# Kernel tuning notes

Measured on AMD Instinct MI355X. Metric: run time of the kernel, lower is better.

Reference implementation:

```python
import jax, jax.numpy as jnp
import numpy as np

D_MODEL = 768
N_HEAD = 12
N_KV_HEADS = 4
HEAD_DIM = D_MODEL // N_HEAD
N_REPEAT = N_HEAD // N_KV_HEADS
ROPE_BASE = 10000.0


def _rotate_half(x):
    # Faithful to the torch impl: reshape(..., 2, d/2) -> transpose(-2,-1) -> reshape
    # (interleaves the two halves), then chunk and cat(-x2, x1).
    d = x.shape[-1]
    xh = x.reshape(*x.shape[:-1], 2, d // 2).swapaxes(-2, -1).reshape(x.shape)
    x1, x2 = jnp.split(xh, 2, axis=-1)
    return jnp.concatenate([-x2, x1], axis=-1)


def _rope(x, pos):
    # x: [B, h, T, d], pos: [T] int
    d = x.shape[-1]
    inv_freq = 1.0 / (ROPE_BASE ** (jnp.arange(0, d, 2, dtype=jnp.float32) / d))
    freqs = pos.astype(jnp.float32)[:, None] * inv_freq[None, :]      # [T, d/2]
    emb = jnp.concatenate([freqs, freqs], axis=-1)                     # [T, d]
    cos = jnp.cos(emb)[None, None]                                     # [1,1,T,d]
    sin = jnp.sin(emb)[None, None]
    xf = x.astype(jnp.float32)
    return (xf * cos + _rotate_half(xf) * sin).astype(x.dtype)


def setup_inputs() -> dict:
    key = jax.random.key(0)
    ks = jax.random.split(key, 6)
    B, T, C = 8, 1024, D_MODEL
    s = 0.02
    return {
        "x": jax.random.normal(ks[0], (B, T, C), dtype=jnp.float32),
        "pos": jnp.arange(T, dtype=jnp.int32),
        "q_w": jax.random.normal(ks[1], (C, N_HEAD * HEAD_DIM), dtype=jnp.float32) * s,
        "q_b": jnp.zeros((N_HEAD * HEAD_DIM,), dtype=jnp.float32),
        "k_w": jax.random.normal(ks[2], (C, N_KV_HEADS * HEAD_DIM), dtype=jnp.float32) * s,
        "k_b": jnp.zeros((N_KV_HEADS * HEAD_DIM,), dtype=jnp.float32),
        "v_w": jax.random.normal(ks[3], (C, N_KV_HEADS * HEAD_DIM), dtype=jnp.float32) * s,
        "v_b": jnp.zeros((N_KV_HEADS * HEAD_DIM,), dtype=jnp.float32),
        "o_w": jax.random.normal(ks[4], (C, C), dtype=jnp.float32) * s,
        "o_b": jnp.zeros((C,), dtype=jnp.float32),
    }


def reference(x, pos, q_w, q_b, k_w, k_b, v_w, v_b, o_w, o_b):
    B, T, C = x.shape
    hd, H, KVH, rep = HEAD_DIM, N_HEAD, N_KV_HEADS, N_REPEAT

    Q = (x @ q_w + q_b).reshape(B, T, H, hd).transpose(0, 2, 1, 3)     # [B,H,T,hd]
    K = (x @ k_w + k_b).reshape(B, T, KVH, hd).transpose(0, 2, 1, 3)   # [B,KVH,T,hd]
    V = (x @ v_w + v_b).reshape(B, T, KVH, hd).transpose(0, 2, 1, 3)

    Q = _rope(Q, pos)
    K = _rope(K, pos)

    # Grouped attention: avoid materializing repeated KV (equiv. to repeat_interleave).
    Qg = Q.reshape(B, KVH, rep, T, hd)
    scores = jnp.einsum("bgrtd,bgsd->bgrts", Qg, K) / np.sqrt(hd).astype(np.float32)
    causal = jnp.tril(jnp.ones((T, T), dtype=bool))
    scores = jnp.where(causal, scores, jnp.finfo(scores.dtype).min)
    probs = jax.nn.softmax(scores, axis=-1)
    out = jnp.einsum("bgrts,bgsd->bgrtd", probs, V)                    # [B,KVH,rep,T,hd]
    out = out.reshape(B, H, T, hd).transpose(0, 2, 1, 3).reshape(B, T, C)
    return out @ o_w + o_b
```

## Files before the change

kernel.cpp:

```cpp
#include <hip/hip_runtime.h>
#include <hip/hip_bf16.h>
#include <math.h>

#define BATCH 8
#define SEQ   1024
#define DM    768
#define NHEAD 12
#define KVH   4
#define HD    64
#define REP   3

#define QSCALE 0.18033688011112042f

typedef unsigned short u16;
typedef __attribute__((ext_vector_type(8))) __bf16 bf16x8;
typedef __attribute__((ext_vector_type(4))) float f32x4;
typedef __attribute__((ext_vector_type(4))) unsigned int u32x4;
typedef __attribute__((address_space(1))) const unsigned int gu32_c;
typedef __attribute__((address_space(3))) unsigned int su32;

__device__ __forceinline__ u16 f2bf(float f) {
    unsigned int u = __float_as_uint(f);
    u += 0x7fffu + ((u >> 16) & 1u);
    return (u16)(u >> 16);
}

__global__ __launch_bounds__(256) void cvt_x_k(
    const float* __restrict__ in, u16* __restrict__ o, int n4)
{
    const int i = blockIdx.x * 256 + threadIdx.x;
    if (i >= n4) return;
    const float4 v = ((const float4*)in)[i];
    ushort4 r;
    r.x = f2bf(v.x); r.y = f2bf(v.y); r.z = f2bf(v.z); r.w = f2bf(v.w);
    ((ushort4*)o)[i] = r;
}

__global__ __launch_bounds__(256) void cvt_wqkv_k(
    const float* __restrict__ qw, const float* __restrict__ kw,
    const float* __restrict__ vw, u16* __restrict__ wt)
{
    const int idx = blockIdx.x * 256 + threadIdx.x;
    if (idx >= 1280 * DM) return;
    const int k = idx % DM;
    const int n = idx / DM;
    float v;
    if (n < 768)       v = qw[(size_t)k * 768 + n] * QSCALE;
    else if (n < 1024) v = kw[(size_t)k * 256 + (n - 768)];
    else               v = vw[(size_t)k * 256 + (n - 1024)];
    wt[idx] = f2bf(v);
}

__global__ __launch_bounds__(256) void cvt_wo_k(
    const float* __restrict__ ow, u16* __restrict__ wt)
{
    const int idx = blockIdx.x * 256 + threadIdx.x;
    if (idx >= DM * DM) return;
    const int k = idx % DM;
    const int n = idx / DM;
    wt[idx] = f2bf(ow[(size_t)k * DM + n]);
}

__device__ __forceinline__ void gemm128_body(
    const u16* __restrict__ A, const u16* __restrict__ B,
    int m0, int n0, u16* As, u16* Bs, f32x4 acc[4][4])
{
    const int tid  = threadIdx.x;
    const int lane = tid & 63;
    const int wid  = tid >> 6;
    const int wr = wid >> 1, wc = wid & 1;
    const int lo = lane & 15, hi = lane >> 4;

    const f32x4 z = {0.f, 0.f, 0.f, 0.f};
    #pragma unroll
    for (int i = 0; i < 4; i++)
        #pragma unroll
        for (int j = 0; j < 4; j++)
            acc[i][j] = z;

    for (int kt = 0; kt < DM; kt += 32) {
        #pragma unroll
        for (int r = 0; r < 2; ++r) {
            const int idx  = r * 256 + tid;
            const int row  = idx >> 2;
            const int col  = (idx & 3) << 3;
            const int base = (r * 256 + wid * 64) * 8;
            __builtin_amdgcn_global_load_lds(
                (gu32_c*)&A[(size_t)(m0 + row) * DM + kt + col],
                (su32*)&As[base], 16, 0, 0);
            __builtin_amdgcn_global_load_lds(
                (gu32_c*)&B[(size_t)(n0 + row) * DM + kt + col],
                (su32*)&Bs[base], 16, 0, 0);
        }
        __syncthreads();
        bf16x8 af[4], bfr[4];
        #pragma unroll
        for (int i = 0; i < 4; i++) af[i]  = *(const bf16x8*)&As[(wr * 64 + i * 16 + lo) * 32 + hi * 8];
        #pragma unroll
        for (int j = 0; j < 4; j++) bfr[j] = *(const bf16x8*)&Bs[(wc * 64 + j * 16 + lo) * 32 + hi * 8];
        #pragma unroll
        for (int i = 0; i < 4; i++)
            #pragma unroll
            for (int j = 0; j < 4; j++)
                acc[i][j] = __builtin_amdgcn_mfma_f32_16x16x32_bf16(af[i], bfr[j], acc[i][j], 0, 0, 0);
        __syncthreads();
    }
}

__global__ __launch_bounds__(256) void gemm_qkv(
    const u16* __restrict__ xb, const u16* __restrict__ wt,
    const float* __restrict__ qb, const float* __restrict__ kb,
    const float* __restrict__ vb,
    u16* __restrict__ Q, u16* __restrict__ K, u16* __restrict__ Vt)
{
    __shared__ __align__(16) u16 As[128 * 32];
    __shared__ __align__(16) u16 Bs[128 * 32];
    const int id = (blockIdx.x & 7) * 80 + (blockIdx.x >> 3);
    const int m0 = (id / 10) * 128;
    const int n0 = (id % 10) * 128;
    f32x4 acc[4][4];
    gemm128_body(xb, wt, m0, n0, As, Bs, acc);

    const int tid = threadIdx.x;
    const int lane = tid & 63, wid = tid >> 6;
    const int wr = wid >> 1, wc = wid & 1;
    const int lo = lane & 15, hi = lane >> 4;

    #pragma unroll
    for (int j = 0; j < 4; j++) {
        const int n = n0 + wc * 64 + j * 16 + lo;
        if (n < 1024) {
            u16* outp; int nl, Hcnt; float bias;
            if (n < 768) { outp = Q; nl = n;       Hcnt = NHEAD; bias = qb[n] * QSCALE; }
            else         { outp = K; nl = n - 768; Hcnt = KVH;   bias = kb[nl]; }
            const int head = nl >> 6, d = nl & 63;
            #pragma unroll
            for (int i = 0; i < 4; i++) {
                #pragma unroll
                for (int r = 0; r < 4; r++) {
                    const int m = m0 + wr * 64 + i * 16 + hi * 4 + r;
                    const int b = m >> 10, t = m & 1023;
                    outp[(((size_t)(b * Hcnt + head)) * SEQ + t) * HD + d] =
                        f2bf(acc[i][j][r] + bias);
                }
            }
        } else {
            const int nl = n - 1024;
            const float bias = vb[nl];
            const int head = nl >> 6, d = nl & 63;
            #pragma unroll
            for (int i = 0; i < 4; i++) {
                ushort4 vs;
                vs.x = f2bf(acc[i][j][0] + bias);
                vs.y = f2bf(acc[i][j][1] + bias);
                vs.z = f2bf(acc[i][j][2] + bias);
                vs.w = f2bf(acc[i][j][3] + bias);
                const int m = m0 + wr * 64 + i * 16 + hi * 4;
                const int b = m >> 10, t = m & 1023;
                *(ushort4*)&Vt[(((size_t)(b * KVH + head)) * HD + d) * SEQ + t] = vs;
            }
        }
    }
}

__global__ __launch_bounds__(256) void gemm_oproj(
    const u16* __restrict__ Ab, const u16* __restrict__ wt,
    const float* __restrict__ ob, float* __restrict__ outp)
{
    __shared__ __align__(16) u16 As[128 * 32];
    __shared__ __align__(16) u16 Bs[128 * 32];
    const int id = (blockIdx.x & 7) * 48 + (blockIdx.x >> 3);
    const int m0 = (id / 6) * 128;
    const int n0 = (id % 6) * 128;
    f32x4 acc[4][4];
    gemm128_body(Ab, wt, m0, n0, As, Bs, acc);

    const int tid = threadIdx.x;
    const int lane = tid & 63, wid = tid >> 6;
    const int wr = wid >> 1, wc = wid & 1;
    const int lo = lane & 15, hi = lane >> 4;

    #pragma unroll
    for (int j = 0; j < 4; j++) {
        const int n = n0 + wc * 64 + j * 16 + lo;
        const float bias = ob[n];
        #pragma unroll
        for (int i = 0; i < 4; i++) {
            #pragma unroll
            for (int r = 0; r < 4; r++) {
                const int m = m0 + wr * 64 + i * 16 + hi * 4 + r;
                outp[(size_t)m * DM + n] = acc[i][j][r] + bias;
            }
        }
    }
}

__global__ __launch_bounds__(256) void rope_naive(
    const __hip_bfloat16* __restrict__ Qin, __hip_bfloat16* __restrict__ Qout,
    const __hip_bfloat16* __restrict__ Kin, __hip_bfloat16* __restrict__ Kout,
    const int* __restrict__ pos)
{
    const long long qrows = (long long)BATCH * NHEAD * SEQ;
    const long long krows = (long long)BATCH * KVH * SEQ;
    const long long gid = (long long)blockIdx.x * 256 + threadIdx.x;
    if (gid >= (qrows + krows) * 64) return;
    long long row = gid >> 6;
    const int j = (int)(gid & 63);
    const __hip_bfloat16* in; __hip_bfloat16* outb;
    if (row < qrows) { in = Qin; outb = Qout; }
    else             { in = Kin; outb = Kout; row -= qrows; }
    const int t = (int)(row & (SEQ - 1));

    float p;
    if (pos[1] == 1)                              p = (float)pos[t];
    else if (((const float*)pos)[1] == 1.0f)      p = ((const float*)pos)[t];
    else                                          p = (float)pos[2 * t];

    const float inv = exp2f(-(float)(j & 31) * (13.287712379549449f / 32.0f));
    float sv, cv;
    sincosf(p * inv, &sv, &cv);
    const int partner = (j & 1) * 32 + (j >> 1) + ((j < 32) ? 16 : -16);
    const float sign  = (j < 32) ? -1.0f : 1.0f;
    const float val  = __bfloat162float(in[row * HD + j]);
    const float pv   = __bfloat162float(in[row * HD + partner]);
    outb[row * HD + j] = __float2bfloat16(val * cv + sign * pv * sv);
}

__device__ __forceinline__ void strip_compute(
    const bf16x8& qf0, const bf16x8& qf1,
    const bf16x8& k0, const bf16x8& k1, const bf16x8& k2, const bf16x8& k3,
    const bf16x8* vv, bool diag, int msk0, int hi,
    float& m, float& l, f32x4* O)
{
    const f32x4 z = {0.f, 0.f, 0.f, 0.f};
    f32x4 a0 = z, a1 = z;
    __builtin_amdgcn_s_setprio(1);
    a0 = __builtin_amdgcn_mfma_f32_16x16x32_bf16(k0, qf0, a0, 0, 0, 0);
    a0 = __builtin_amdgcn_mfma_f32_16x16x32_bf16(k1, qf1, a0, 0, 0, 0);
    a1 = __builtin_amdgcn_mfma_f32_16x16x32_bf16(k2, qf0, a1, 0, 0, 0);
    a1 = __builtin_amdgcn_mfma_f32_16x16x32_bf16(k3, qf1, a1, 0, 0, 0);
    __builtin_amdgcn_s_setprio(0);

    float sc[8];
    #pragma unroll
    for (int e = 0; e < 8; ++e)
        sc[e] = (e < 4) ? a0[e & 3] : a1[e & 3];
    if (diag) {
        #pragma unroll
        for (int e = 0; e < 8; ++e) {
            const int srel = ((e >> 2) << 4) + (hi << 2) + (e & 3);
            if (srel > msk0) sc[e] = -3.0e38f;
        }
    }
    float pm = sc[0];
    #pragma unroll
    for (int e = 1; e < 8; ++e) pm = fmaxf(pm, sc[e]);

    if (!__all(pm - m <= 8.0f)) {
        float pr = fmaxf(pm, __shfl_xor(pm, 16));
        pr = fmaxf(pr, __shfl_xor(pr, 32));
        const float mn = fmaxf(m, pr);
        const float f = exp2f(m - mn);
        l *= f;
        #pragma unroll
        for (int r = 0; r < 4; ++r) {
            const float fr = __shfl(f, hi * 4 + r);
            #pragma unroll
            for (int dj = 0; dj < 4; ++dj) O[dj][r] *= fr;
        }
        m = mn;
    }

    union { u16 u[8]; bf16x8 v; } pu;
    float ps = 0.f;
    #pragma unroll
    for (int e = 0; e < 8; ++e) {
        const float p = exp2f(sc[e] - m);
        ps += p;
        pu.u[e] = f2bf(p);
    }
    l += ps;

    __builtin_amdgcn_s_setprio(1);
    #pragma unroll
    for (int dj = 0; dj < 4; ++dj)
        O[dj] = __builtin_amdgcn_mfma_f32_16x16x32_bf16(pu.v, vv[dj], O[dj], 0, 0, 0);
    __builtin_amdgcn_s_setprio(0);
}

__global__ __launch_bounds__(256, 2) void attn_mfma(
    const u16* __restrict__ Q, const u16* __restrict__ K,
    const u16* __restrict__ Vt, u16* __restrict__ outp)
{
    __shared__ __align__(16) u16 Ks[2][2048];
    __shared__ __align__(16) u16 Vs[2][2048];

    const int wg = (blockIdx.x & 7) * 96 + (blockIdx.x >> 3);
    const int bh = wg >> 3;
    const int c  = wg & 7;
    const int b  = bh / NHEAD, h = bh % NHEAD;
    const int g  = h / REP;
    const int wid  = threadIdx.x >> 6;
    const int lane = threadIdx.x & 63;
    const int lo = lane & 15, hi = lane >> 4;

    const int w    = c + (wid << 3);
    const int sA   = 63 - w, sB = w;
    const int dA   = sA >> 1, dB = sB >> 1;
    const int mskA = lo + ((sA & 1) << 4);
    const int mskB = lo + ((sB & 1) << 4);
    const int nstT = ((63 - c) >> 1) + 1;

    const u16* Kp = K  + (size_t)(b * KVH + g) * SEQ * HD;
    const u16* Vp = Vt + (size_t)(b * KVH + g) * SEQ * HD;

    const int jK = (wid << 6) + lane;
    const int sKoff = (jK ^ ((jK >> 3) & 7)) << 3;
    int vsoff[4];
    #pragma unroll
    for (int q = 0; q < 4; ++q) {
        const int dw  = (wid << 8) + (q << 6) + lane;
        const int R   = dw >> 4;
        const int wd  = dw & 15;
        const int c8p = wd >> 1, ii = wd & 1;
        const int sc8 = (c8p >> 1) + ((c8p & 1) << 2);
        vsoff[q] = (R << 10) + (((sc8 << 1) + ii) << 1);
    }

    const u16* QpA = Q + ((size_t)(b * NHEAD + h) * SEQ + (sA << 4)) * HD;
    const u16* QpB = Q + ((size_t)(b * NHEAD + h) * SEQ + (sB << 4)) * HD;
    const bf16x8 qA0 = *(const bf16x8*)&QpA[(size_t)lo * HD + hi * 8];
    const bf16x8 qA1 = *(const bf16x8*)&QpA[(size_t)lo * HD + 32 + hi * 8];
    const bf16x8 qB0 = *(const bf16x8*)&QpB[(size_t)lo * HD + hi * 8];
    const bf16x8 qB1 = *(const bf16x8*)&QpB[(size_t)lo * HD + 32 + hi * 8];

    const f32x4 z = {0.f, 0.f, 0.f, 0.f};
    f32x4 OA[4], OB[4];
    #pragma unroll
    for (int dj = 0; dj < 4; ++dj) { OA[dj] = z; OB[dj] = z; }
    float mA = -3.0e38f, lA = 0.f, mB = -3.0e38f, lB = 0.f;

    #define STAGE(st_, bf_) do {                                              \
        const int s0_ = (st_) << 5;                                           \
        __builtin_amdgcn_global_load_lds(                                     \
            (gu32_c*)(Kp + (s0_ << 6) + sKoff),                               \
            (su32*)&Ks[bf_][wid << 9], 16, 0, 0);                             \
        _Pragma("unroll")                                                     \
        for (int q_ = 0; q_ < 4; ++q_)                                        \
            __builtin_amdgcn_global_load_lds(                                 \
                (gu32_c*)(Vp + s0_ + vsoff[q_]),                              \
                (su32*)&Vs[bf_][(wid << 9) + (q_ << 7)], 4, 0, 0);            \
    } while (0)

    STAGE(0, 0);
    __syncthreads();

    const int xorK = lo & 7;
    for (int st = 0; st < nstT; ++st) {
        const int buf = st & 1;
        if (st + 1 < nstT) STAGE(st + 1, buf ^ 1);

        if (st <= dA) {
            const u16* kb_ = Ks[buf];
            const bf16x8 k0 = *(const bf16x8*)&kb_[((lo << 3) + (hi ^ xorK)) << 3];
            const bf16x8 k1 = *(const bf16x8*)&kb_[((lo << 3) + ((4 + hi) ^ xorK)) << 3];
            const bf16x8 k2 = *(const bf16x8*)&kb_[(((16 + lo) << 3) + (hi ^ xorK)) << 3];
            const bf16x8 k3 = *(const bf16x8*)&kb_[(((16 + lo) << 3) + ((4 + hi) ^ xorK)) << 3];
            bf16x8 vv[4];
            #pragma unroll
            for (int dj = 0; dj < 4; ++dj)
                vv[dj] = *(const bf16x8*)&Vs[buf][((dj * 16 + lo) << 5) + (hi << 3)];

            strip_compute(qA0, qA1, k0, k1, k2, k3, vv, st == dA, mskA, hi, mA, lA, OA);
            if (st <= dB)
                strip_compute(qB0, qB1, k0, k1, k2, k3, vv, st == dB, mskB, hi, mB, lB, OB);
        }
        __syncthreads();
    }
    #undef STAGE

    lA += __shfl_xor(lA, 16); lA += __shfl_xor(lA, 32);
    lB += __shfl_xor(lB, 16); lB += __shfl_xor(lB, 32);
    #pragma unroll
    for (int r = 0; r < 4; ++r) {
        const float liA = 1.0f / fmaxf(__shfl(lA, hi * 4 + r), 1e-37f);
        const float liB = 1.0f / fmaxf(__shfl(lB, hi * 4 + r), 1e-37f);
        const int tA = (sA << 4) + hi * 4 + r;
        const int tB = (sB << 4) + hi * 4 + r;
        #pragma unroll
        for (int dj = 0; dj < 4; ++dj) {
            outp[((size_t)(b * SEQ + tA)) * DM + h * HD + dj * 16 + lo] = f2bf(OA[dj][r] * liA);
            outp[((size_t)(b * SEQ + tB)) * DM + h * HD + dj * 16 + lo] = f2bf(OB[dj][r] * liB);
        }
    }
}

extern "C" void kernel_launch(void* const* d_in, const int* in_sizes, int n_in,
                              void* d_out, int out_size, void* d_ws, size_t ws_size,
                              hipStream_t stream) {
    const float* x   = (const float*)d_in[0];
    const int*   pos = (const int*)d_in[1];
    const float* qw  = (const float*)d_in[2];
    const float* qb  = (const float*)d_in[3];
    const float* kw  = (const float*)d_in[4];
    const float* kb  = (const float*)d_in[5];
    const float* vw  = (const float*)d_in[6];
    const float* vb  = (const float*)d_in[7];
    const float* ow  = (const float*)d_in[8];
    const float* ob  = (const float*)d_in[9];
    float* out = (float*)d_out;

    u16* xb    = (u16*)d_ws;
    u16* Wqkvt = xb    + (size_t)8192 * DM;
    u16* Wot   = Wqkvt + (size_t)1280 * DM;
    u16* Qbuf  = Wot   + (size_t)DM * DM;
    u16* Kbuf  = Qbuf  + (size_t)BATCH * NHEAD * SEQ * HD;
    u16* Krot  = Kbuf  + (size_t)BATCH * KVH * SEQ * HD;
    u16* Vtb   = Krot  + (size_t)BATCH * KVH * SEQ * HD;
    u16* Qrot  = xb;
    u16* attn  = Qbuf;

    cvt_x_k<<<(8192 * DM / 4 + 255) / 256, 256, 0, stream>>>(x, xb, 8192 * DM / 4);
    cvt_wqkv_k<<<(1280 * DM + 255) / 256, 256, 0, stream>>>(qw, kw, vw, Wqkvt);
    cvt_wo_k<<<(DM * DM + 255) / 256, 256, 0, stream>>>(ow, Wot);

    gemm_qkv<<<640, 256, 0, stream>>>(xb, Wqkvt, qb, kb, vb, Qbuf, Kbuf, Vtb);

    const long long allrows = (long long)BATCH * (NHEAD + KVH) * SEQ;
    rope_naive<<<(int)((allrows * 64 + 255) / 256), 256, 0, stream>>>(
        (const __hip_bfloat16*)Qbuf, (__hip_bfloat16*)Qrot,
        (const __hip_bfloat16*)Kbuf, (__hip_bfloat16*)Krot, pos);

    attn_mfma<<<96 * 8, 256, 0, stream>>>(Qrot, Krot, Vtb, attn);

    gemm_oproj<<<384, 256, 0, stream>>>(attn, Wot, ob, out);
}
```

Before: 233.3 us.

## Split attention into one strip per wave, add separate V transpose kernel

The attention kernel now gives each wave a single 16-row query strip instead of a balanced pair. It launches twice as many workgroups with a higher occupancy hint (4 blocks/CU) and applies an XOR swizzle to the V shared-memory layout to reduce bank conflicts. The QKV GEMM now writes V in row layout into the Krot buffer, and a new transpose kernel produces Vt, replacing the strided ushort4 scatter stores. This trades causal load balancing and an extra launch plus V round-trip for more parallelism, better occupancy and coalesced stores.

```diff
diff --git a/kernel.cpp b/kernel.cpp
--- a/kernel.cpp
+++ b/kernel.cpp
@@ -111,7 +111,7 @@
     const u16* __restrict__ xb, const u16* __restrict__ wt,
     const float* __restrict__ qb, const float* __restrict__ kb,
     const float* __restrict__ vb,
-    u16* __restrict__ Q, u16* __restrict__ K, u16* __restrict__ Vt)
+    u16* __restrict__ Q, u16* __restrict__ K, u16* __restrict__ Vr)
 {
     __shared__ __align__(16) u16 As[128 * 32];
     __shared__ __align__(16) u16 Bs[128 * 32];
@@ -129,38 +129,48 @@
     #pragma unroll
     for (int j = 0; j < 4; j++) {
         const int n = n0 + wc * 64 + j * 16 + lo;
-        if (n < 1024) {
-            u16* outp; int nl, Hcnt; float bias;
-            if (n < 768) { outp = Q; nl = n;       Hcnt = NHEAD; bias = qb[n] * QSCALE; }
-            else         { outp = K; nl = n - 768; Hcnt = KVH;   bias = kb[nl]; }
-            const int head = nl >> 6, d = nl & 63;
+        u16* outp; int nl, Hcnt; float bias;
+        if (n < 768)       { outp = Q;  nl = n;        Hcnt = NHEAD; bias = qb[n] * QSCALE; }
+        else if (n < 1024) { outp = K;  nl = n - 768;  Hcnt = KVH;   bias = kb[nl]; }
+        else               { outp = Vr; nl = n - 1024; Hcnt = KVH;   bias = vb[nl]; }
+        const int head = nl >> 6, d = nl & 63;
+        #pragma unroll
+        for (int i = 0; i < 4; i++) {
             #pragma unroll
-            for (int i = 0; i < 4; i++) {
-                #pragma unroll
-                for (int r = 0; r < 4; r++) {
-                    const int m = m0 + wr * 64 + i * 16 + hi * 4 + r;
-                    const int b = m >> 10, t = m & 1023;
-                    outp[(((size_t)(b * Hcnt + head)) * SEQ + t) * HD + d] =
-                        f2bf(acc[i][j][r] + bias);
-                }
+            for (int r = 0; r < 4; r++) {
+                const int m = m0 + wr * 64 + i * 16 + hi * 4 + r;
+                const int b = m >> 10, t = m & 1023;
+                outp[(((size_t)(b * Hcnt + head)) * SEQ + t) * HD + d] =
+                    f2bf(acc[i][j][r] + bias);
             }
-        } else {
-            const int nl = n - 1024;
-            const float bias = vb[nl];
-            const int head = nl >> 6, d = nl & 63;
-            #pragma unroll
-            for (int i = 0; i < 4; i++) {
-                ushort4 vs;
-                vs.x = f2bf(acc[i][j][0] + bias);
-                vs.y = f2bf(acc[i][j][1] + bias);
-                vs.z = f2bf(acc[i][j][2] + bias);
-                vs.w = f2bf(acc[i][j][3] + bias);
-                const int m = m0 + wr * 64 + i * 16 + hi * 4;
-                const int b = m >> 10, t = m & 1023;
-                *(ushort4*)&Vt[(((size_t)(b * KVH + head)) * HD + d) * SEQ + t] = vs;
-            }
-        }
-    }
+        }
+    }
+}
+
+__global__ __launch_bounds__(256) void vtrans_k(
+    const u16* __restrict__ in, u16* __restrict__ out)
+{
+    __shared__ u16 T[64][72];
+    const int blk = blockIdx.x;
+    const int bg  = blk >> 4;
+    const int t0  = (blk & 15) << 6;
+    const int tid = threadIdx.x;
+    const int tl  = tid & 63;
+    const int d0  = (tid >> 6) << 4;
+
+    union { u32x4 v[2]; u16 u[16]; } ld;
+    const u16* src = in + ((size_t)bg * SEQ + t0 + tl) * HD + d0;
+    ld.v[0] = *(const u32x4*)(src);
+    ld.v[1] = *(const u32x4*)(src + 8);
+    #pragma unroll
+    for (int k = 0; k < 16; ++k) T[d0 + k][tl] = ld.u[k];
+    __syncthreads();
+
+    const int d  = tid >> 2;
+    const int tc = (tid & 3) << 4;
+    u16* dst = out + ((size_t)bg * HD + d) * SEQ + t0 + tc;
+    *(u32x4*)(dst)     = *(const u32x4*)&T[d][tc];
+    *(u32x4*)(dst + 8) = *(const u32x4*)&T[d][tc + 8];
 }
 
 __global__ __launch_bounds__(256) void gemm_oproj(
@@ -288,28 +298,27 @@
     __builtin_amdgcn_s_setprio(0);
 }
 
-__global__ __launch_bounds__(256, 2) void attn_mfma(
+__global__ __launch_bounds__(256, 4) void attn_mfma(
     const u16* __restrict__ Q, const u16* __restrict__ K,
     const u16* __restrict__ Vt, u16* __restrict__ outp)
 {
     __shared__ __align__(16) u16 Ks[2][2048];
     __shared__ __align__(16) u16 Vs[2][2048];
 
-    const int wg = (blockIdx.x & 7) * 96 + (blockIdx.x >> 3);
-    const int bh = wg >> 3;
-    const int c  = wg & 7;
+    const int wg = (blockIdx.x & 7) * 192 + (blockIdx.x >> 3);
+    const int bh = wg >> 4;
+    const int c  = wg & 15;
     const int b  = bh / NHEAD, h = bh % NHEAD;
     const int g  = h / REP;
     const int wid  = threadIdx.x >> 6;
     const int lane = threadIdx.x & 63;
     const int lo = lane & 15, hi = lane >> 4;
 
-    const int w    = c + (wid << 3);
-    const int sA   = 63 - w, sB = w;
-    const int dA   = sA >> 1, dB = sB >> 1;
-    const int mskA = lo + ((sA & 1) << 4);
-    const int mskB = lo + ((sB & 1) << 4);
-    const int nstT = ((63 - c) >> 1) + 1;
+    const int w    = c + (wid << 4);
+    const int q0   = w << 4;
+    const int dT   = w >> 1;
+    const int msk0 = lo + ((w & 1) << 4);
+    const int nstT = ((c + 48) >> 1) + 1;
 
     const u16* Kp = K  + (size_t)(b * KVH + g) * SEQ * HD;
     const u16* Vp = Vt + (size_t)(b * KVH + g) * SEQ * HD;
@@ -322,23 +331,19 @@
         const int dw  = (wid << 8) + (q << 6) + lane;
         const int R   = dw >> 4;
         const int wd  = dw & 15;
-        const int c8p = wd >> 1, ii = wd & 1;
-        const int sc8 = (c8p >> 1) + ((c8p & 1) << 2);
-        vsoff[q] = (R << 10) + (((sc8 << 1) + ii) << 1);
-    }
-
-    const u16* QpA = Q + ((size_t)(b * NHEAD + h) * SEQ + (sA << 4)) * HD;
-    const u16* QpB = Q + ((size_t)(b * NHEAD + h) * SEQ + (sB << 4)) * HD;
-    const bf16x8 qA0 = *(const bf16x8*)&QpA[(size_t)lo * HD + hi * 8];
-    const bf16x8 qA1 = *(const bf16x8*)&QpA[(size_t)lo * HD + 32 + hi * 8];
-    const bf16x8 qB0 = *(const bf16x8*)&QpB[(size_t)lo * HD + hi * 8];
-    const bf16x8 qB1 = *(const bf16x8*)&QpB[(size_t)lo * HD + 32 + hi * 8];
+        const int hpl = (wd >> 2) ^ ((R >> 1) & 3);
+        vsoff[q] = (R << 10) + (hpl << 2) + (((wd >> 1) & 1) << 4) + ((wd & 1) << 1);
+    }
+
+    const u16* Qp = Q + ((size_t)(b * NHEAD + h) * SEQ + q0) * HD;
+    const bf16x8 qf0 = *(const bf16x8*)&Qp[(size_t)lo * HD + hi * 8];
+    const bf16x8 qf1 = *(const bf16x8*)&Qp[(size_t)lo * HD + 32 + hi * 8];
 
     const f32x4 z = {0.f, 0.f, 0.f, 0.f};
-    f32x4 OA[4], OB[4];
-    #pragma unroll
-    for (int dj = 0; dj < 4; ++dj) { OA[dj] = z; OB[dj] = z; }
-    float mA = -3.0e38f, lA = 0.f, mB = -3.0e38f, lB = 0.f;
+    f32x4 O[4];
+    #pragma unroll
+    for (int dj = 0; dj < 4; ++dj) O[dj] = z;
+    float m = -3.0e38f, l = 0.f;
 
     #define STAGE(st_, bf_) do {                                              \
         const int s0_ = (st_) << 5;                                           \
@@ -360,7 +365,7 @@
         const int buf = st & 1;
         if (st + 1 < nstT) STAGE(st + 1, buf ^ 1);
 
-        if (st <= dA) {
+        if (st <= dT) {
             const u16* kb_ = Ks[buf];
             const bf16x8 k0 = *(const bf16x8*)&kb_[((lo << 3) + (hi ^ xorK)) << 3];
             const bf16x8 k1 = *(const bf16x8*)&kb_[((lo << 3) + ((4 + hi) ^ xorK)) << 3];
@@ -368,30 +373,24 @@
             const bf16x8 k3 = *(const bf16x8*)&kb_[(((16 + lo) << 3) + ((4 + hi) ^ xorK)) << 3];
             bf16x8 vv[4];
             #pragma unroll
-            for (int dj = 0; dj < 4; ++dj)
-                vv[dj] = *(const bf16x8*)&Vs[buf][((dj * 16 + lo) << 5) + (hi << 3)];
-
-            strip_compute(qA0, qA1, k0, k1, k2, k3, vv, st == dA, mskA, hi, mA, lA, OA);
-            if (st <= dB)
-                strip_compute(qB0, qB1, k0, k1, k2, k3, vv, st == dB, mskB, hi, mB, lB, OB);
+            for (int dj = 0; dj < 4; ++dj) {
+                const int R = dj * 16 + lo;
+                vv[dj] = *(const bf16x8*)&Vs[buf][(R << 5) + ((hi ^ ((R >> 1) & 3)) << 3)];
+            }
+            strip_compute(qf0, qf1, k0, k1, k2, k3, vv, st == dT, msk0, hi, m, l, O);
         }
         __syncthreads();
     }
     #undef STAGE
 
-    lA += __shfl_xor(lA, 16); lA += __shfl_xor(lA, 32);
-    lB += __shfl_xor(lB, 16); lB += __shfl_xor(lB, 32);
+    l += __shfl_xor(l, 16); l += __shfl_xor(l, 32);
     #pragma unroll
     for (int r = 0; r < 4; ++r) {
-        const float liA = 1.0f / fmaxf(__shfl(lA, hi * 4 + r), 1e-37f);
-        const float liB = 1.0f / fmaxf(__shfl(lB, hi * 4 + r), 1e-37f);
-        const int tA = (sA << 4) + hi * 4 + r;
-        const int tB = (sB << 4) + hi * 4 + r;
-        #pragma unroll
-        for (int dj = 0; dj < 4; ++dj) {
-            outp[((size_t)(b * SEQ + tA)) * DM + h * HD + dj * 16 + lo] = f2bf(OA[dj][r] * liA);
-            outp[((size_t)(b * SEQ + tB)) * DM + h * HD + dj * 16 + lo] = f2bf(OB[dj][r] * liB);
-        }
+        const float li = 1.0f / fmaxf(__shfl(l, hi * 4 + r), 1e-37f);
+        const int t = q0 + hi * 4 + r;
+        #pragma unroll
+        for (int dj = 0; dj < 4; ++dj)
+            outp[((size_t)(b * SEQ + t)) * DM + h * HD + dj * 16 + lo] = f2bf(O[dj][r] * li);
     }
 }
 
@@ -419,19 +418,22 @@
     u16* Vtb   = Krot  + (size_t)BATCH * KVH * SEQ * HD;
     u16* Qrot  = xb;
     u16* attn  = Qbuf;
+    u16* Vraw  = Krot;
 
     cvt_x_k<<<(8192 * DM / 4 + 255) / 256, 256, 0, stream>>>(x, xb, 8192 * DM / 4);
     cvt_wqkv_k<<<(1280 * DM + 255) / 256, 256, 0, stream>>>(qw, kw, vw, Wqkvt);
     cvt_wo_k<<<(DM * DM + 255) / 256, 256, 0, stream>>>(ow, Wot);
 
-    gemm_qkv<<<640, 256, 0, stream>>>(xb, Wqkvt, qb, kb, vb, Qbuf, Kbuf, Vtb);
+    gemm_qkv<<<640, 256, 0, stream>>>(xb, Wqkvt, qb, kb, vb, Qbuf, Kbuf, Vraw);
+
+    vtrans_k<<<512, 256, 0, stream>>>(Vraw, Vtb);
 
     const long long allrows = (long long)BATCH * (NHEAD + KVH) * SEQ;
     rope_naive<<<(int)((allrows * 64 + 255) / 256), 256, 0, stream>>>(
         (const __hip_bfloat16*)Qbuf, (__hip_bfloat16*)Qrot,
         (const __hip_bfloat16*)Kbuf, (__hip_bfloat16*)Krot, pos);
 
-    attn_mfma<<<96 * 8, 256, 0, stream>>>(Qrot, Krot, Vtb, attn);
+    attn_mfma<<<96 * 16, 256, 0, stream>>>(Qrot, Krot, Vtb, attn);
 
     gemm_oproj<<<384, 256, 0, stream>>>(attn, Wot, ob, out);
 }
```

Measured after the change: 232.7 us. About the same (-0.2%).

## Quad-buffer GEMM and attention LDS loads; add separate V transpose kernel

Applied to the files above, without the earlier changes.

The shared GEMM body and the attention kernel now use four LDS slots with loads issued two iterations ahead. A vmcnt wait plus a raw barrier replaces the two __syncthreads per iteration, so global-to-LDS copies overlap with MFMA work. The QKV GEMM now writes V in row layout, and a new tiled transpose kernel produces the transposed V the attention kernel expects. Attention's V LDS layout gains an XOR swizzle to reduce bank conflicts. The cost is more LDS per block, which may lower occupancy, plus an extra kernel launch and an extra pass over V in memory.

```diff
diff --git a/kernel.cpp b/kernel.cpp
--- a/kernel.cpp
+++ b/kernel.cpp
@@ -63,7 +63,7 @@
 
 __device__ __forceinline__ void gemm128_body(
     const u16* __restrict__ A, const u16* __restrict__ B,
-    int m0, int n0, u16* As, u16* Bs, f32x4 acc[4][4])
+    int m0, int n0, u16 (*As)[4096], u16 (*Bs)[4096], f32x4 acc[4][4])
 {
     const int tid  = threadIdx.x;
     const int lane = tid & 63;
@@ -78,43 +78,57 @@
         for (int j = 0; j < 4; j++)
             acc[i][j] = z;
 
-    for (int kt = 0; kt < DM; kt += 32) {
-        #pragma unroll
-        for (int r = 0; r < 2; ++r) {
-            const int idx  = r * 256 + tid;
-            const int row  = idx >> 2;
-            const int col  = (idx & 3) << 3;
-            const int base = (r * 256 + wid * 64) * 8;
-            __builtin_amdgcn_global_load_lds(
-                (gu32_c*)&A[(size_t)(m0 + row) * DM + kt + col],
-                (su32*)&As[base], 16, 0, 0);
-            __builtin_amdgcn_global_load_lds(
-                (gu32_c*)&B[(size_t)(n0 + row) * DM + kt + col],
-                (su32*)&Bs[base], 16, 0, 0);
-        }
-        __syncthreads();
+    const int NT = DM / 32;
+
+    #define STAGE_G(kt_, sl_) do {                                            \
+        _Pragma("unroll")                                                     \
+        for (int r_ = 0; r_ < 2; ++r_) {                                      \
+            const int idx_  = r_ * 256 + tid;                                 \
+            const int row_  = idx_ >> 2;                                      \
+            const int col_  = (idx_ & 3) << 3;                                \
+            const int base_ = (r_ * 256 + wid * 64) * 8;                      \
+            __builtin_amdgcn_global_load_lds(                                 \
+                (gu32_c*)&A[(size_t)(m0 + row_) * DM + (kt_) * 32 + col_],    \
+                (su32*)&As[sl_][base_], 16, 0, 0);                            \
+            __builtin_amdgcn_global_load_lds(                                 \
+                (gu32_c*)&B[(size_t)(n0 + row_) * DM + (kt_) * 32 + col_],    \
+                (su32*)&Bs[sl_][base_], 16, 0, 0);                            \
+        }                                                                     \
+    } while (0)
+
+    STAGE_G(0, 0);
+    STAGE_G(1, 1);
+
+    for (int kt = 0; kt < NT; ++kt) {
+        const int k2 = (kt + 2 < NT) ? kt + 2 : NT - 1;
+        STAGE_G(k2, (kt + 2) & 3);
+        asm volatile("s_waitcnt vmcnt(8)" ::: "memory");
+        __builtin_amdgcn_s_barrier();
+        __builtin_amdgcn_sched_barrier(0);
+
+        const int sl = kt & 3;
         bf16x8 af[4], bfr[4];
         #pragma unroll
-        for (int i = 0; i < 4; i++) af[i]  = *(const bf16x8*)&As[(wr * 64 + i * 16 + lo) * 32 + hi * 8];
-        #pragma unroll
-        for (int j = 0; j < 4; j++) bfr[j] = *(const bf16x8*)&Bs[(wc * 64 + j * 16 + lo) * 32 + hi * 8];
+        for (int i = 0; i < 4; i++) af[i]  = *(const bf16x8*)&As[sl][(wr * 64 + i * 16 + lo) * 32 + hi * 8];
+        #pragma unroll
+        for (int j = 0; j < 4; j++) bfr[j] = *(const bf16x8*)&Bs[sl][(wc * 64 + j * 16 + lo) * 32 + hi * 8];
         #pragma unroll
         for (int i = 0; i < 4; i++)
             #pragma unroll
             for (int j = 0; j < 4; j++)
                 acc[i][j] = __builtin_amdgcn_mfma_f32_16x16x32_bf16(af[i], bfr[j], acc[i][j], 0, 0, 0);
-        __syncthreads();
-    }
+    }
+    #undef STAGE_G
 }
 
 __global__ __launch_bounds__(256) void gemm_qkv(
     const u16* __restrict__ xb, const u16* __restrict__ wt,
     const float* __restrict__ qb, const float* __restrict__ kb,
     const float* __restrict__ vb,
-    u16* __restrict__ Q, u16* __restrict__ K, u16* __restrict__ Vt)
-{
-    __shared__ __align__(16) u16 As[128 * 32];
-    __shared__ __align__(16) u16 Bs[128 * 32];
+    u16* __restrict__ Q, u16* __restrict__ K, u16* __restrict__ Vr)
+{
+    __shared__ __align__(16) u16 As[4][4096];
+    __shared__ __align__(16) u16 Bs[4][4096];
     const int id = (blockIdx.x & 7) * 80 + (blockIdx.x >> 3);
     const int m0 = (id / 10) * 128;
     const int n0 = (id % 10) * 128;
@@ -129,46 +143,56 @@
     #pragma unroll
     for (int j = 0; j < 4; j++) {
         const int n = n0 + wc * 64 + j * 16 + lo;
-        if (n < 1024) {
-            u16* outp; int nl, Hcnt; float bias;
-            if (n < 768) { outp = Q; nl = n;       Hcnt = NHEAD; bias = qb[n] * QSCALE; }
-            else         { outp = K; nl = n - 768; Hcnt = KVH;   bias = kb[nl]; }
-            const int head = nl >> 6, d = nl & 63;
+        u16* outp; int nl, Hcnt; float bias;
+        if (n < 768)       { outp = Q;  nl = n;        Hcnt = NHEAD; bias = qb[n] * QSCALE; }
+        else if (n < 1024) { outp = K;  nl = n - 768;  Hcnt = KVH;   bias = kb[nl]; }
+        else               { outp = Vr; nl = n - 1024; Hcnt = KVH;   bias = vb[nl]; }
+        const int head = nl >> 6, d = nl & 63;
+        #pragma unroll
+        for (int i = 0; i < 4; i++) {
             #pragma unroll
-            for (int i = 0; i < 4; i++) {
-                #pragma unroll
-                for (int r = 0; r < 4; r++) {
-                    const int m = m0 + wr * 64 + i * 16 + hi * 4 + r;
-                    const int b = m >> 10, t = m & 1023;
-                    outp[(((size_t)(b * Hcnt + head)) * SEQ + t) * HD + d] =
-                        f2bf(acc[i][j][r] + bias);
-                }
+            for (int r = 0; r < 4; r++) {
+                const int m = m0 + wr * 64 + i * 16 + hi * 4 + r;
+                const int b = m >> 10, t = m & 1023;
+                outp[(((size_t)(b * Hcnt + head)) * SEQ + t) * HD + d] =
+                    f2bf(acc[i][j][r] + bias);
             }
-        } else {
-            const int nl = n - 1024;
-            const float bias = vb[nl];
-            const int head = nl >> 6, d = nl & 63;
-            #pragma unroll
-            for (int i = 0; i < 4; i++) {
-                ushort4 vs;
-                vs.x = f2bf(acc[i][j][0] + bias);
-                vs.y = f2bf(acc[i][j][1] + bias);
-                vs.z = f2bf(acc[i][j][2] + bias);
-                vs.w = f2bf(acc[i][j][3] + bias);
-                const int m = m0 + wr * 64 + i * 16 + hi * 4;
-                const int b = m >> 10, t = m & 1023;
-                *(ushort4*)&Vt[(((size_t)(b * KVH + head)) * HD + d) * SEQ + t] = vs;
-            }
-        }
-    }
+        }
+    }
+}
+
+__global__ __launch_bounds__(256) void vtrans_k(
+    const u16* __restrict__ in, u16* __restrict__ out)
+{
+    __shared__ u16 T[64][72];
+    const int blk = blockIdx.x;
+    const int bg  = blk >> 4;
+    const int t0  = (blk & 15) << 6;
+    const int tid = threadIdx.x;
+    const int tl  = tid & 63;
+    const int d0  = (tid >> 6) << 4;
+
+    union { u32x4 v[2]; u16 u[16]; } ld;
+    const u16* src = in + ((size_t)bg * SEQ + t0 + tl) * HD + d0;
+    ld.v[0] = *(const u32x4*)(src);
+    ld.v[1] = *(const u32x4*)(src + 8);
+    #pragma unroll
+    for (int k = 0; k < 16; ++k) T[d0 + k][tl] = ld.u[k];
+    __syncthreads();
+
+    const int d  = tid >> 2;
+    const int tc = (tid & 3) << 4;
+    u16* dst = out + ((size_t)bg * HD + d) * SEQ + t0 + tc;
+    *(u32x4*)(dst)     = *(const u32x4*)&T[d][tc];
+    *(u32x4*)(dst + 8) = *(const u32x4*)&T[d][tc + 8];
 }
 
 __global__ __launch_bounds__(256) void gemm_oproj(
     const u16* __restrict__ Ab, const u16* __restrict__ wt,
     const float* __restrict__ ob, float* __restrict__ outp)
 {
-    __shared__ __align__(16) u16 As[128 * 32];
-    __shared__ __align__(16) u16 Bs[128 * 32];
+    __shared__ __align__(16) u16 As[4][4096];
+    __shared__ __align__(16) u16 Bs[4][4096];
     const int id = (blockIdx.x & 7) * 48 + (blockIdx.x >> 3);
     const int m0 = (id / 6) * 128;
     const int n0 = (id % 6) * 128;
@@ -292,8 +316,8 @@
     const u16* __restrict__ Q, const u16* __restrict__ K,
     const u16* __restrict__ Vt, u16* __restrict__ outp)
 {
-    __shared__ __align__(16) u16 Ks[2][2048];
-    __shared__ __align__(16) u16 Vs[2][2048];
+    __shared__ __align__(16) u16 Ks[4][2048];
+    __shared__ __align__(16) u16 Vs[4][2048];
 
     const int wg = (blockIdx.x & 7) * 96 + (blockIdx.x >> 3);
     const int bh = wg >> 3;
@@ -322,9 +346,8 @@
         const int dw  = (wid << 8) + (q << 6) + lane;
         const int R   = dw >> 4;
         const int wd  = dw & 15;
-        const int c8p = wd >> 1, ii = wd & 1;
-        const int sc8 = (c8p >> 1) + ((c8p & 1) << 2);
-        vsoff[q] = (R << 10) + (((sc8 << 1) + ii) << 1);
+        const int hpl = (wd >> 2) ^ ((R >> 1) & 3);
+        vsoff[q] = (R << 10) + (hpl << 2) + (((wd >> 1) & 1) << 4) + ((wd & 1) << 1);
     }
 
     const u16* QpA = Q + ((size_t)(b * NHEAD + h) * SEQ + (sA << 4)) * HD;
@@ -340,42 +363,46 @@
     for (int dj = 0; dj < 4; ++dj) { OA[dj] = z; OB[dj] = z; }
     float mA = -3.0e38f, lA = 0.f, mB = -3.0e38f, lB = 0.f;
 
-    #define STAGE(st_, bf_) do {                                              \
+    #define STAGE(st_, sl_) do {                                              \
         const int s0_ = (st_) << 5;                                           \
         __builtin_amdgcn_global_load_lds(                                     \
             (gu32_c*)(Kp + (s0_ << 6) + sKoff),                               \
-            (su32*)&Ks[bf_][wid << 9], 16, 0, 0);                             \
+            (su32*)&Ks[sl_][wid << 9], 16, 0, 0);                             \
         _Pragma("unroll")                                                     \
         for (int q_ = 0; q_ < 4; ++q_)                                        \
             __builtin_amdgcn_global_load_lds(                                 \
                 (gu32_c*)(Vp + s0_ + vsoff[q_]),                              \
-                (su32*)&Vs[bf_][(wid << 9) + (q_ << 7)], 4, 0, 0);            \
+                (su32*)&Vs[sl_][(wid << 9) + (q_ << 7)], 4, 0, 0);            \
     } while (0)
 
     STAGE(0, 0);
-    __syncthreads();
+    STAGE(1, 1);
 
     const int xorK = lo & 7;
     for (int st = 0; st < nstT; ++st) {
-        const int buf = st & 1;
-        if (st + 1 < nstT) STAGE(st + 1, buf ^ 1);
+        const int s2 = (st + 2 < nstT) ? st + 2 : nstT - 1;
+        STAGE(s2, (st + 2) & 3);
+        asm volatile("s_waitcnt vmcnt(10)" ::: "memory");
+        __builtin_amdgcn_s_barrier();
+        __builtin_amdgcn_sched_barrier(0);
 
         if (st <= dA) {
-            const u16* kb_ = Ks[buf];
+            const int sl = st & 3;
+            const u16* kb_ = Ks[sl];
             const bf16x8 k0 = *(const bf16x8*)&kb_[((lo << 3) + (hi ^ xorK)) << 3];
             const bf16x8 k1 = *(const bf16x8*)&kb_[((lo << 3) + ((4 + hi) ^ xorK)) << 3];
             const bf16x8 k2 = *(const bf16x8*)&kb_[(((16 + lo) << 3) + (hi ^ xorK)) << 3];
             const bf16x8 k3 = *(const bf16x8*)&kb_[(((16 + lo) << 3) + ((4 + hi) ^ xorK)) << 3];
             bf16x8 vv[4];
             #pragma unroll
-            for (int dj = 0; dj < 4; ++dj)
-                vv[dj] = *(const bf16x8*)&Vs[buf][((dj * 16 + lo) << 5) + (hi << 3)];
-
+            for (int dj = 0; dj < 4; ++dj) {
+                const int R = dj * 16 + lo;
+                vv[dj] = *(const bf16x8*)&Vs[sl][(R << 5) + ((hi ^ ((R >> 1) & 3)) << 3)];
+            }
             strip_compute(qA0, qA1, k0, k1, k2, k3, vv, st == dA, mskA, hi, mA, lA, OA);
             if (st <= dB)
                 strip_compute(qB0, qB1, k0, k1, k2, k3, vv, st == dB, mskB, hi, mB, lB, OB);
         }
-        __syncthreads();
     }
     #undef STAGE
 
@@ -419,12 +446,15 @@
     u16* Vtb   = Krot  + (size_t)BATCH * KVH * SEQ * HD;
     u16* Qrot  = xb;
     u16* attn  = Qbuf;
+    u16* Vraw  = Krot;
 
     cvt_x_k<<<(8192 * DM / 4 + 255) / 256, 256, 0, stream>>>(x, xb, 8192 * DM / 4);
     cvt_wqkv_k<<<(1280 * DM + 255) / 256, 256, 0, stream>>>(qw, kw, vw, Wqkvt);
     cvt_wo_k<<<(DM * DM + 255) / 256, 256, 0, stream>>>(ow, Wot);
 
-    gemm_qkv<<<640, 256, 0, stream>>>(xb, Wqkvt, qb, kb, vb, Qbuf, Kbuf, Vtb);
+    gemm_qkv<<<640, 256, 0, stream>>>(xb, Wqkvt, qb, kb, vb, Qbuf, Kbuf, Vraw);
+
+    vtrans_k<<<512, 256, 0, stream>>>(Vraw, Vtb);
 
     const long long allrows = (long long)BATCH * (NHEAD + KVH) * SEQ;
     rope_naive<<<(int)((allrows * 64 + 255) / 256), 256, 0, stream>>>(
```

New measurement: 229.8 us. About the same (-1.5%).
